# Kernel optimization log

Measured on AMD Instinct MI355X. Metric: run time of the kernel, lower is better.

The kernel has to match this reference:

```python
import jax, jax.numpy as jnp
import numpy as np

B, S, L = 256, 512, 128


def setup_inputs() -> dict:
    key = jax.random.key(0)
    k0, k1, k2, k3, k4, k5 = jax.random.split(key, 6)
    features = jax.random.normal(k0, (B, S, L), dtype=jnp.float32)
    attention_mask = jnp.ones((B, S), dtype=jnp.int32)  # all positions valid
    labels = jax.random.randint(k1, (B, S), 0, L)
    confidence = jax.random.uniform(k2, (B,), dtype=jnp.float32)
    start_transitions = jax.random.uniform(k3, (L,), minval=-0.1, maxval=0.1)
    end_transitions = jax.random.uniform(k4, (L,), minval=-0.1, maxval=0.1)
    transitions = jax.random.uniform(k5, (L, L), minval=-0.1, maxval=0.1)
    return {
        "features": features,
        "start_transitions": start_transitions,
        "end_transitions": end_transitions,
        "transitions": transitions,
        "confidence": confidence,
        "attention_mask": attention_mask,
        "labels": labels,
    }


def _crf_loss(features, start_transitions, end_transitions, transitions,
              confidence, attention_mask, labels):
    # time-major, matching torch.swapaxes(features, 0, 1)
    feats = jnp.swapaxes(features, 0, 1)                    # [S,B,L]
    mask = jnp.swapaxes(attention_mask, 0, 1).astype(bool)  # [S,B]
    labs = jnp.swapaxes(jnp.where(labels == -100, 0, labels), 0, 1)  # [S,B]
    bs = feats.shape[1]
    barange = jnp.arange(bs)

    # ---- log numerator (gold path score), fully vectorized over time ----
    emit = jnp.take_along_axis(feats, labs[:, :, None], axis=2)[..., 0]  # [S,B]
    trans_scores = transitions[labs[:-1], labs[1:]]                      # [S-1,B]
    maskf = mask[1:].astype(feats.dtype)
    log_num = (start_transitions[labs[0]] + emit[0]
               + jnp.sum((trans_scores + emit[1:]) * maskf, axis=0))
    seq_lens = mask.sum(axis=0) - 1                                      # [B]
    last_tags = labs[seq_lens, barange]
    log_num = log_num + end_transitions[last_tags]

    # ---- log denominator (partition function) via sequential scan ----
    def step(alpha, xs):
        feat_t, mask_t = xs  # [B,L], [B]
        nxt = jax.nn.logsumexp(
            alpha[:, :, None] + transitions[None, :, :] + feat_t[:, None, :],
            axis=1)
        return jnp.where(mask_t[:, None], nxt, alpha), None

    alpha0 = start_transitions + feats[0]                    # [B,L]
    alpha, _ = jax.lax.scan(step, alpha0, (feats[1:], mask[1:]))
    log_den = jax.nn.logsumexp(alpha + end_transitions, axis=1)  # [B]

    loss = (log_den - log_num) * confidence
    return jnp.mean(loss)


def reference(features, start_transitions, end_transitions, transitions,
              confidence, attention_mask, labels):
    return _crf_loss(features, start_transitions, end_transitions, transitions,
                     confidence, attention_mask, labels)
```

## Files before the change

kernel.cpp:

```cpp
#include <hip/hip_runtime.h>
#include <hip/hip_bf16.h>
#include <math.h>

#define NB 256
#define SS 512
#define LL 128

typedef short bf16x8 __attribute__((ext_vector_type(8)));
typedef float f32x4 __attribute__((ext_vector_type(4)));

__device__ __forceinline__ short f2bf(float f) {
    __hip_bfloat16 h = __float2bfloat16(f);
    short s;
    __builtin_memcpy(&s, &h, 2);
    return s;
}
__device__ __forceinline__ float bf2f(short s) {
    return __int_as_float(((int)(unsigned short)s) << 16);
}

#define MFMA1632(c, a, bb) \
    c = __builtin_amdgcn_mfma_f32_16x16x32_bf16(a, bb, c, 0, 0, 0)

__device__ __forceinline__ void wave_barrier() {
    asm volatile("s_waitcnt lgkmcnt(0)" ::: "memory");
    __builtin_amdgcn_s_barrier();
}

template <int ISB>
__device__ __forceinline__ void run_chain4(
    const int w, const int lane,
    const float* __restrict__ fb,
    const float* __restrict__ start_t,
    const float* __restrict__ end_t,
    const float* __restrict__ trans,
    short* __restrict__ img,
    float* __restrict__ eRing,
    const int* __restrict__ lmask,
    float* __restrict__ outv,
    float* __restrict__ oute)
{
    const int lo = lane & 15;
    const int hi = lane >> 4;
    const int nt0 = 2 * w, nt1 = 2 * w + 1;

    bf16x8 Af0[4], Af1[4];
#pragma unroll
    for (int kt = 0; kt < 4; ++kt) {
        bf16x8 f0, f1;
        const int n0 = 16 * nt0 + lo, n1 = 16 * nt1 + lo;
#pragma unroll
        for (int j = 0; j < 8; ++j) {
            const int k = 32 * kt + 8 * hi + j;
            f0[j] = f2bf(__expf(ISB ? trans[n0 * LL + k] : trans[k * LL + n0]));
            f1[j] = f2bf(__expf(ISB ? trans[n1 * LL + k] : trans[k * LL + n1]));
        }
        Af0[kt] = f0;
        Af1[kt] = f1;
    }

    float v[2][4];
#pragma unroll
    for (int n2 = 0; n2 < 2; ++n2)
#pragma unroll
        for (int j = 0; j < 4; ++j) {
            const int p = 16 * (2 * w + n2) + 4 * hi + j;
            v[n2][j] = ISB ? __expf(end_t[p]) : __expf(start_t[p] + fb[p]);
        }

    short4 pk0, pk1;
    {
        f32x4 e0 = {1.f, 1.f, 1.f, 1.f}, e1 = e0;
        if (ISB) {
#pragma unroll
            for (int j = 0; j < 4; ++j) {
                e0[j] = __expf(fb[(size_t)511 * LL + 16 * nt0 + 4 * hi + j]);
                e1[j] = __expf(fb[(size_t)511 * LL + 16 * nt1 + 4 * hi + j]);
            }
        }
        pk0.x = f2bf(v[0][0] * e0[0]); pk0.y = f2bf(v[0][1] * e0[1]);
        pk0.z = f2bf(v[0][2] * e0[2]); pk0.w = f2bf(v[0][3] * e0[3]);
        pk1.x = f2bf(v[1][0] * e1[0]); pk1.y = f2bf(v[1][1] * e1[1]);
        pk1.z = f2bf(v[1][2] * e1[2]); pk1.w = f2bf(v[1][3] * e1[3]);
    }

    float2 nxt;
    {
        const int row = ISB ? (508 - w) : (w + 3);
        nxt = *(const float2*)(fb + (size_t)row * LL + 2 * lane);
    }

    wave_barrier();

    int eacc = 0;

    for (int r = 0; r < 256; ++r) {
        short* ib = img + (r & 1) * LL;

        if (lo == 0) {
            *(short4*)(ib + 32 * w + 4 * hi) = pk0;
            *(short4*)(ib + 32 * w + 16 + 4 * hi) = pk1;
        }
        const float* rp = eRing + (r & 3) * LL + 4 * hi;
        f32x4 ec0 = *(const f32x4*)(rp + 16 * nt0);
        f32x4 ec1 = *(const f32x4*)(rp + 16 * nt1);
        if (w == (r & 3)) {
            *(float2*)(eRing + ((r + 2) & 3) * LL + 2 * lane) =
                make_float2(__expf(nxt.x), __expf(nxt.y));
            const int rowN = ISB ? (504 - r) : (r + 7);
            nxt = *(const float2*)(fb + (size_t)rowN * LL + 2 * lane);
        }
        int mt = lmask[ISB ? (511 - r) : (r + 1)];
        if (!ISB && r == 255) mt = 0;

        wave_barrier();

        __builtin_amdgcn_s_setprio(1);
        bf16x8 Bf[4];
#pragma unroll
        for (int kt = 0; kt < 4; ++kt)
            Bf[kt] = *(const bf16x8*)(ib + 32 * kt + 8 * hi);

        f32x4 c0a = {0.f, 0.f, 0.f, 0.f}, c0b = c0a, c1a = c0a, c1b = c0a;
        MFMA1632(c0a, Af0[0], Bf[0]);
        MFMA1632(c1a, Af1[0], Bf[0]);
        MFMA1632(c0b, Af0[2], Bf[2]);
        MFMA1632(c1b, Af1[2], Bf[2]);
        MFMA1632(c0a, Af0[1], Bf[1]);
        MFMA1632(c1a, Af1[1], Bf[1]);
        MFMA1632(c0b, Af0[3], Bf[3]);
        MFMA1632(c1b, Af1[3], Bf[3]);
        __builtin_amdgcn_s_setprio(0);
        const f32x4 cc0 = c0a + c0b;
        const f32x4 cc1 = c1a + c1b;

#pragma unroll
        for (int j = 0; j < 4; ++j) {
            const float c0 = ISB ? cc0[j] : ec0[j] * cc0[j];
            const float c1 = ISB ? cc1[j] : ec1[j] * cc1[j];
            v[0][j] = mt ? c0 : v[0][j];
            v[1][j] = mt ? c1 : v[1][j];
        }

        if ((r & 7) == 7) {
            float s = 0.f;
#pragma unroll
            for (int kt = 0; kt < 4; ++kt)
#pragma unroll
                for (int j = 0; j < 8; ++j) s += bf2f(Bf[kt][j]);
            s += __shfl_xor(s, 16);
            s += __shfl_xor(s, 32);
            int ex;
            frexpf(s, &ex);
#pragma unroll
            for (int n2 = 0; n2 < 2; ++n2)
#pragma unroll
                for (int j = 0; j < 4; ++j) v[n2][j] = ldexpf(v[n2][j], -ex);
            eacc += ex;
        }

        pk0.x = f2bf(ISB ? v[0][0] * ec0[0] : v[0][0]);
        pk0.y = f2bf(ISB ? v[0][1] * ec0[1] : v[0][1]);
        pk0.z = f2bf(ISB ? v[0][2] * ec0[2] : v[0][2]);
        pk0.w = f2bf(ISB ? v[0][3] * ec0[3] : v[0][3]);
        pk1.x = f2bf(ISB ? v[1][0] * ec1[0] : v[1][0]);
        pk1.y = f2bf(ISB ? v[1][1] * ec1[1] : v[1][1]);
        pk1.z = f2bf(ISB ? v[1][2] * ec1[2] : v[1][2]);
        pk1.w = f2bf(ISB ? v[1][3] * ec1[3] : v[1][3]);
    }

    if (lo == 0) {
        *(f32x4*)(outv + 16 * nt0 + 4 * hi) =
            (f32x4){v[0][0], v[0][1], v[0][2], v[0][3]};
        *(f32x4*)(outv + 16 * nt1 + 4 * hi) =
            (f32x4){v[1][0], v[1][1], v[1][2], v[1][3]};
    }
    if (w == 0 && lane == 0) *oute = (float)eacc;
}

__global__ __launch_bounds__(256, 2) void crf_chain_kernel(
    const float* __restrict__ feats,
    const float* __restrict__ start_t,
    const float* __restrict__ end_t,
    const float* __restrict__ trans,
    const int* __restrict__ mask,
    const int* __restrict__ labels,
    float* __restrict__ ws)
{
    const int bid = blockIdx.x;
    const int b = bid & 255;
    const int isB = bid >> 8;
    const int tid = threadIdx.x;
    const int w = tid >> 6;
    const int lane = tid & 63;

    __shared__ __align__(16) short img[2 * LL];
    __shared__ __align__(16) float eRing[4 * LL];
    __shared__ int lmask[SS];
    __shared__ float nred[4];
    __shared__ int cred[4];

    const float* fb = feats + (size_t)b * SS * LL;

    lmask[tid] = mask[b * SS + tid];
    lmask[tid + 256] = mask[b * SS + tid + 256];
    {
        const int slot = tid >> 7;
        const int e = tid & 127;
        const int row = isB ? (510 - slot) : (1 + slot);
        eRing[slot * LL + e] = __expf(fb[(size_t)row * LL + e]);
    }

    float* av = ws;
    float* bv = ws + NB * LL;
    float* eFa = ws + 2 * NB * LL;
    float* eBa = eFa + NB;
    float* lognum = eBa + NB;

    if (isB)
        run_chain4<1>(w, lane, fb, start_t, end_t, trans, img, eRing, lmask,
                      bv + b * LL, eBa + b);
    else
        run_chain4<0>(w, lane, fb, start_t, end_t, trans, img, eRing, lmask,
                      av + b * LL, eFa + b);

    if (isB) {
        const int* lb = labels + b * SS;
        const int* mb = mask + b * SS;
        float term = 0.f;
        int cnt = 0;
#pragma unroll
        for (int q = 0; q < 2; ++q) {
            const int tt = tid + 256 * q;
            int l = lb[tt];
            if ((unsigned)l >= LL) l = 0;
            const int m = mb[tt];
            cnt += (m != 0);
            if (tt == 0) {
                term += start_t[l] + fb[l];
            } else if (m) {
                int lp = lb[tt - 1];
                if ((unsigned)lp >= LL) lp = 0;
                term += trans[lp * LL + l] + fb[(size_t)tt * LL + l];
            }
        }
#pragma unroll
        for (int o = 1; o < 64; o <<= 1) {
            term += __shfl_xor(term, o);
            cnt += __shfl_xor(cnt, o);
        }
        if (lane == 0) { nred[w] = term; cred[w] = cnt; }
        __syncthreads();
        if (tid == 0) {
            const float tot = nred[0] + nred[1] + nred[2] + nred[3];
            const int c = cred[0] + cred[1] + cred[2] + cred[3];
            int sl = c - 1;
            sl = sl < 0 ? 0 : (sl >= SS ? SS - 1 : sl);
            int lt = lb[sl];
            if ((unsigned)lt >= LL) lt = 0;
            lognum[b] = tot + end_t[lt];
        }
    }
}

__global__ __launch_bounds__(256) void crf_final_kernel(
    const float* __restrict__ ws, const float* __restrict__ conf,
    float* __restrict__ out)
{
    const int tid = threadIdx.x;
    const float* av = ws;
    const float* bv = ws + NB * LL;
    const float* eFa = ws + 2 * NB * LL;
    const float* eBa = eFa + NB;
    const float* ln = eBa + NB;

    const float4* a4 = (const float4*)(av + tid * LL);
    const float4* b4 = (const float4*)(bv + tid * LL);
    float dot = 0.f;
#pragma unroll 8
    for (int k = 0; k < 32; ++k) {
        float4 a = a4[k], bb = b4[k];
        dot += a.x * bb.x + a.y * bb.y + a.z * bb.z + a.w * bb.w;
    }
    float logZ = logf(dot) + 0.69314718055994531f * (eFa[tid] + eBa[tid]);
    float loss = (logZ - ln[tid]) * conf[tid] * (1.0f / NB);

#pragma unroll
    for (int o = 1; o < 64; o <<= 1) loss += __shfl_xor(loss, o);
    __shared__ float red[4];
    if ((tid & 63) == 0) red[tid >> 6] = loss;
    __syncthreads();
    if (tid == 0) out[0] = red[0] + red[1] + red[2] + red[3];
}

extern "C" void kernel_launch(void* const* d_in, const int* in_sizes, int n_in,
                              void* d_out, int out_size, void* d_ws, size_t ws_size,
                              hipStream_t stream) {
    const float* feats  = (const float*)d_in[0];
    const float* startt = (const float*)d_in[1];
    const float* endt   = (const float*)d_in[2];
    const float* trans  = (const float*)d_in[3];
    const float* conf   = (const float*)d_in[4];
    const int*   mask   = (const int*)d_in[5];
    const int*   labels = (const int*)d_in[6];
    float* out = (float*)d_out;
    float* ws = (float*)d_ws;

    hipLaunchKernelGGL(crf_chain_kernel, dim3(2 * NB), dim3(256), 0, stream,
                       feats, startt, endt, trans, mask, labels, ws);
    hipLaunchKernelGGL(crf_final_kernel, dim3(1), dim3(256), 0, stream,
                       ws, conf, out);
}
```

Before: 214.8 us.

## Interleave two batch chains per block to hide the serial step latency

Each block now runs two independent sequences (a pair of batch items) in lockstep and alternates their scan steps. While one chain's MFMA result and bf16 repack are in flight, the other chain's LDS image is read, so the latency of each serial step is hidden. The grid is halved to 256 blocks with launch bounds of one block per SM. The transition matrix is loaded once and shared by both chains, but register pressure rises and each block does twice the serial work.

```diff
diff --git a/kernel.cpp b/kernel.cpp
--- a/kernel.cpp
+++ b/kernel.cpp
@@ -28,17 +28,22 @@
 }
 
 template <int ISB>
-__device__ __forceinline__ void run_chain4(
+__device__ __forceinline__ void run_pair(
     const int w, const int lane,
-    const float* __restrict__ fb,
+    const float* __restrict__ fb0,
+    const float* __restrict__ fb1,
     const float* __restrict__ start_t,
     const float* __restrict__ end_t,
     const float* __restrict__ trans,
-    short* __restrict__ img,
-    float* __restrict__ eRing,
-    const int* __restrict__ lmask,
+    short* __restrict__ imgA,
+    short* __restrict__ imgB,
+    float* __restrict__ ringA,
+    float* __restrict__ ringB,
+    const int* __restrict__ lmA,
+    const int* __restrict__ lmB,
     float* __restrict__ outv,
-    float* __restrict__ oute)
+    float* __restrict__ oute,
+    const int b0, const int b1)
 {
     const int lo = lane & 15;
     const int hi = lane >> 4;
@@ -59,89 +64,98 @@
         Af1[kt] = f1;
     }
 
-    float v[2][4];
+    float vA[2][4], vB[2][4];
 #pragma unroll
     for (int n2 = 0; n2 < 2; ++n2)
 #pragma unroll
         for (int j = 0; j < 4; ++j) {
             const int p = 16 * (2 * w + n2) + 4 * hi + j;
-            v[n2][j] = ISB ? __expf(end_t[p]) : __expf(start_t[p] + fb[p]);
-        }
-
-    short4 pk0, pk1;
+            vA[n2][j] = ISB ? __expf(end_t[p]) : __expf(start_t[p] + fb0[p]);
+            vB[n2][j] = ISB ? __expf(end_t[p]) : __expf(start_t[p] + fb1[p]);
+        }
+
+    short4 pkA0, pkA1, pkB0, pkB1;
     {
-        f32x4 e0 = {1.f, 1.f, 1.f, 1.f}, e1 = e0;
+        f32x4 eA0 = {1.f, 1.f, 1.f, 1.f}, eA1 = eA0, eB0 = eA0, eB1 = eA0;
         if (ISB) {
 #pragma unroll
             for (int j = 0; j < 4; ++j) {
-                e0[j] = __expf(fb[(size_t)511 * LL + 16 * nt0 + 4 * hi + j]);
-                e1[j] = __expf(fb[(size_t)511 * LL + 16 * nt1 + 4 * hi + j]);
-            }
-        }
-        pk0.x = f2bf(v[0][0] * e0[0]); pk0.y = f2bf(v[0][1] * e0[1]);
-        pk0.z = f2bf(v[0][2] * e0[2]); pk0.w = f2bf(v[0][3] * e0[3]);
-        pk1.x = f2bf(v[1][0] * e1[0]); pk1.y = f2bf(v[1][1] * e1[1]);
-        pk1.z = f2bf(v[1][2] * e1[2]); pk1.w = f2bf(v[1][3] * e1[3]);
-    }
-
-    float2 nxt;
+                eA0[j] = __expf(fb0[(size_t)511 * LL + 16 * nt0 + 4 * hi + j]);
+                eA1[j] = __expf(fb0[(size_t)511 * LL + 16 * nt1 + 4 * hi + j]);
+                eB0[j] = __expf(fb1[(size_t)511 * LL + 16 * nt0 + 4 * hi + j]);
+                eB1[j] = __expf(fb1[(size_t)511 * LL + 16 * nt1 + 4 * hi + j]);
+            }
+        }
+        pkA0.x = f2bf(vA[0][0] * eA0[0]); pkA0.y = f2bf(vA[0][1] * eA0[1]);
+        pkA0.z = f2bf(vA[0][2] * eA0[2]); pkA0.w = f2bf(vA[0][3] * eA0[3]);
+        pkA1.x = f2bf(vA[1][0] * eA1[0]); pkA1.y = f2bf(vA[1][1] * eA1[1]);
+        pkA1.z = f2bf(vA[1][2] * eA1[2]); pkA1.w = f2bf(vA[1][3] * eA1[3]);
+        pkB0.x = f2bf(vB[0][0] * eB0[0]); pkB0.y = f2bf(vB[0][1] * eB0[1]);
+        pkB0.z = f2bf(vB[0][2] * eB0[2]); pkB0.w = f2bf(vB[0][3] * eB0[3]);
+        pkB1.x = f2bf(vB[1][0] * eB1[0]); pkB1.y = f2bf(vB[1][1] * eB1[1]);
+        pkB1.z = f2bf(vB[1][2] * eB1[2]); pkB1.w = f2bf(vB[1][3] * eB1[3]);
+    }
+
+    if (lo == 0) {
+        *(short4*)(imgA + 32 * w + 4 * hi) = pkA0;
+        *(short4*)(imgA + 32 * w + 16 + 4 * hi) = pkA1;
+    }
+
+    float2 nxtA, nxtB;
     {
         const int row = ISB ? (508 - w) : (w + 3);
-        nxt = *(const float2*)(fb + (size_t)row * LL + 2 * lane);
-    }
-
-    wave_barrier();
-
-    int eacc = 0;
+        nxtA = *(const float2*)(fb0 + (size_t)row * LL + 2 * lane);
+        nxtB = *(const float2*)(fb1 + (size_t)row * LL + 2 * lane);
+    }
+
+    int eaccA = 0, eaccB = 0;
 
     for (int r = 0; r < 256; ++r) {
-        short* ib = img + (r & 1) * LL;
-
-        if (lo == 0) {
-            *(short4*)(ib + 32 * w + 4 * hi) = pk0;
-            *(short4*)(ib + 32 * w + 16 + 4 * hi) = pk1;
-        }
-        const float* rp = eRing + (r & 3) * LL + 4 * hi;
-        f32x4 ec0 = *(const f32x4*)(rp + 16 * nt0);
-        f32x4 ec1 = *(const f32x4*)(rp + 16 * nt1);
+        wave_barrier();
+        const short* ibA = imgA + (r & 1) * LL;
+        bf16x8 Bf[4];
+#pragma unroll
+        for (int kt = 0; kt < 4; ++kt)
+            Bf[kt] = *(const bf16x8*)(ibA + 32 * kt + 8 * hi);
+        {
+            short* ob = imgB + (r & 1) * LL;
+            if (lo == 0) {
+                *(short4*)(ob + 32 * w + 4 * hi) = pkB0;
+                *(short4*)(ob + 32 * w + 16 + 4 * hi) = pkB1;
+            }
+        }
+        const float* rpA = ringA + (r & 3) * LL + 4 * hi;
+        f32x4 ecA0 = *(const f32x4*)(rpA + 16 * nt0);
+        f32x4 ecA1 = *(const f32x4*)(rpA + 16 * nt1);
         if (w == (r & 3)) {
-            *(float2*)(eRing + ((r + 2) & 3) * LL + 2 * lane) =
-                make_float2(__expf(nxt.x), __expf(nxt.y));
+            *(float2*)(ringA + ((r + 2) & 3) * LL + 2 * lane) =
+                make_float2(__expf(nxtA.x), __expf(nxtA.y));
             const int rowN = ISB ? (504 - r) : (r + 7);
-            nxt = *(const float2*)(fb + (size_t)rowN * LL + 2 * lane);
-        }
-        int mt = lmask[ISB ? (511 - r) : (r + 1)];
-        if (!ISB && r == 255) mt = 0;
-
-        wave_barrier();
-
-        __builtin_amdgcn_s_setprio(1);
-        bf16x8 Bf[4];
-#pragma unroll
-        for (int kt = 0; kt < 4; ++kt)
-            Bf[kt] = *(const bf16x8*)(ib + 32 * kt + 8 * hi);
-
-        f32x4 c0a = {0.f, 0.f, 0.f, 0.f}, c0b = c0a, c1a = c0a, c1b = c0a;
-        MFMA1632(c0a, Af0[0], Bf[0]);
-        MFMA1632(c1a, Af1[0], Bf[0]);
-        MFMA1632(c0b, Af0[2], Bf[2]);
-        MFMA1632(c1b, Af1[2], Bf[2]);
-        MFMA1632(c0a, Af0[1], Bf[1]);
-        MFMA1632(c1a, Af1[1], Bf[1]);
-        MFMA1632(c0b, Af0[3], Bf[3]);
-        MFMA1632(c1b, Af1[3], Bf[3]);
-        __builtin_amdgcn_s_setprio(0);
-        const f32x4 cc0 = c0a + c0b;
-        const f32x4 cc1 = c1a + c1b;
-
-#pragma unroll
-        for (int j = 0; j < 4; ++j) {
-            const float c0 = ISB ? cc0[j] : ec0[j] * cc0[j];
-            const float c1 = ISB ? cc1[j] : ec1[j] * cc1[j];
-            v[0][j] = mt ? c0 : v[0][j];
-            v[1][j] = mt ? c1 : v[1][j];
-        }
-
+            nxtA = *(const float2*)(fb0 + (size_t)rowN * LL + 2 * lane);
+        }
+        int mtA = lmA[ISB ? (511 - r) : (r + 1)];
+        if (!ISB && r == 255) mtA = 0;
+
+        {
+            f32x4 c0a = {0.f, 0.f, 0.f, 0.f}, c0b = c0a, c1a = c0a, c1b = c0a;
+            MFMA1632(c0a, Af0[0], Bf[0]);
+            MFMA1632(c1a, Af1[0], Bf[0]);
+            MFMA1632(c0b, Af0[2], Bf[2]);
+            MFMA1632(c1b, Af1[2], Bf[2]);
+            MFMA1632(c0a, Af0[1], Bf[1]);
+            MFMA1632(c1a, Af1[1], Bf[1]);
+            MFMA1632(c0b, Af0[3], Bf[3]);
+            MFMA1632(c1b, Af1[3], Bf[3]);
+            const f32x4 cc0 = c0a + c0b;
+            const f32x4 cc1 = c1a + c1b;
+#pragma unroll
+            for (int j = 0; j < 4; ++j) {
+                const float c0 = ISB ? cc0[j] : ecA0[j] * cc0[j];
+                const float c1 = ISB ? cc1[j] : ecA1[j] * cc1[j];
+                vA[0][j] = mtA ? c0 : vA[0][j];
+                vA[1][j] = mtA ? c1 : vA[1][j];
+            }
+        }
         if ((r & 7) == 7) {
             float s = 0.f;
 #pragma unroll
@@ -155,30 +169,106 @@
 #pragma unroll
             for (int n2 = 0; n2 < 2; ++n2)
 #pragma unroll
-                for (int j = 0; j < 4; ++j) v[n2][j] = ldexpf(v[n2][j], -ex);
-            eacc += ex;
-        }
-
-        pk0.x = f2bf(ISB ? v[0][0] * ec0[0] : v[0][0]);
-        pk0.y = f2bf(ISB ? v[0][1] * ec0[1] : v[0][1]);
-        pk0.z = f2bf(ISB ? v[0][2] * ec0[2] : v[0][2]);
-        pk0.w = f2bf(ISB ? v[0][3] * ec0[3] : v[0][3]);
-        pk1.x = f2bf(ISB ? v[1][0] * ec1[0] : v[1][0]);
-        pk1.y = f2bf(ISB ? v[1][1] * ec1[1] : v[1][1]);
-        pk1.z = f2bf(ISB ? v[1][2] * ec1[2] : v[1][2]);
-        pk1.w = f2bf(ISB ? v[1][3] * ec1[3] : v[1][3]);
+                for (int j = 0; j < 4; ++j) vA[n2][j] = ldexpf(vA[n2][j], -ex);
+            eaccA += ex;
+        }
+        pkA0.x = f2bf(ISB ? vA[0][0] * ecA0[0] : vA[0][0]);
+        pkA0.y = f2bf(ISB ? vA[0][1] * ecA0[1] : vA[0][1]);
+        pkA0.z = f2bf(ISB ? vA[0][2] * ecA0[2] : vA[0][2]);
+        pkA0.w = f2bf(ISB ? vA[0][3] * ecA0[3] : vA[0][3]);
+        pkA1.x = f2bf(ISB ? vA[1][0] * ecA1[0] : vA[1][0]);
+        pkA1.y = f2bf(ISB ? vA[1][1] * ecA1[1] : vA[1][1]);
+        pkA1.z = f2bf(ISB ? vA[1][2] * ecA1[2] : vA[1][2]);
+        pkA1.w = f2bf(ISB ? vA[1][3] * ecA1[3] : vA[1][3]);
+
+        wave_barrier();
+        const short* ibB = imgB + (r & 1) * LL;
+        bf16x8 Bg[4];
+#pragma unroll
+        for (int kt = 0; kt < 4; ++kt)
+            Bg[kt] = *(const bf16x8*)(ibB + 32 * kt + 8 * hi);
+        {
+            short* ob = imgA + ((r + 1) & 1) * LL;
+            if (lo == 0) {
+                *(short4*)(ob + 32 * w + 4 * hi) = pkA0;
+                *(short4*)(ob + 32 * w + 16 + 4 * hi) = pkA1;
+            }
+        }
+        const float* rpB = ringB + (r & 3) * LL + 4 * hi;
+        f32x4 ecB0 = *(const f32x4*)(rpB + 16 * nt0);
+        f32x4 ecB1 = *(const f32x4*)(rpB + 16 * nt1);
+        if (w == (r & 3)) {
+            *(float2*)(ringB + ((r + 2) & 3) * LL + 2 * lane) =
+                make_float2(__expf(nxtB.x), __expf(nxtB.y));
+            const int rowN = ISB ? (504 - r) : (r + 7);
+            nxtB = *(const float2*)(fb1 + (size_t)rowN * LL + 2 * lane);
+        }
+        int mtB = lmB[ISB ? (511 - r) : (r + 1)];
+        if (!ISB && r == 255) mtB = 0;
+
+        {
+            f32x4 c0a = {0.f, 0.f, 0.f, 0.f}, c0b = c0a, c1a = c0a, c1b = c0a;
+            MFMA1632(c0a, Af0[0], Bg[0]);
+            MFMA1632(c1a, Af1[0], Bg[0]);
+            MFMA1632(c0b, Af0[2], Bg[2]);
+            MFMA1632(c1b, Af1[2], Bg[2]);
+            MFMA1632(c0a, Af0[1], Bg[1]);
+            MFMA1632(c1a, Af1[1], Bg[1]);
+            MFMA1632(c0b, Af0[3], Bg[3]);
+            MFMA1632(c1b, Af1[3], Bg[3]);
+            const f32x4 cc0 = c0a + c0b;
+            const f32x4 cc1 = c1a + c1b;
+#pragma unroll
+            for (int j = 0; j < 4; ++j) {
+                const float c0 = ISB ? cc0[j] : ecB0[j] * cc0[j];
+                const float c1 = ISB ? cc1[j] : ecB1[j] * cc1[j];
+                vB[0][j] = mtB ? c0 : vB[0][j];
+                vB[1][j] = mtB ? c1 : vB[1][j];
+            }
+        }
+        if ((r & 7) == 7) {
+            float s = 0.f;
+#pragma unroll
+            for (int kt = 0; kt < 4; ++kt)
+#pragma unroll
+                for (int j = 0; j < 8; ++j) s += bf2f(Bg[kt][j]);
+            s += __shfl_xor(s, 16);
+            s += __shfl_xor(s, 32);
+            int ex;
+            frexpf(s, &ex);
+#pragma unroll
+            for (int n2 = 0; n2 < 2; ++n2)
+#pragma unroll
+                for (int j = 0; j < 4; ++j) vB[n2][j] = ldexpf(vB[n2][j], -ex);
+            eaccB += ex;
+        }
+        pkB0.x = f2bf(ISB ? vB[0][0] * ecB0[0] : vB[0][0]);
+        pkB0.y = f2bf(ISB ? vB[0][1] * ecB0[1] : vB[0][1]);
+        pkB0.z = f2bf(ISB ? vB[0][2] * ecB0[2] : vB[0][2]);
+        pkB0.w = f2bf(ISB ? vB[0][3] * ecB0[3] : vB[0][3]);
+        pkB1.x = f2bf(ISB ? vB[1][0] * ecB1[0] : vB[1][0]);
+        pkB1.y = f2bf(ISB ? vB[1][1] * ecB1[1] : vB[1][1]);
+        pkB1.z = f2bf(ISB ? vB[1][2] * ecB1[2] : vB[1][2]);
+        pkB1.w = f2bf(ISB ? vB[1][3] * ecB1[3] : vB[1][3]);
     }
 
     if (lo == 0) {
-        *(f32x4*)(outv + 16 * nt0 + 4 * hi) =
-            (f32x4){v[0][0], v[0][1], v[0][2], v[0][3]};
-        *(f32x4*)(outv + 16 * nt1 + 4 * hi) =
-            (f32x4){v[1][0], v[1][1], v[1][2], v[1][3]};
-    }
-    if (w == 0 && lane == 0) *oute = (float)eacc;
-}
-
-__global__ __launch_bounds__(256, 2) void crf_chain_kernel(
+        *(f32x4*)(outv + b0 * LL + 16 * nt0 + 4 * hi) =
+            (f32x4){vA[0][0], vA[0][1], vA[0][2], vA[0][3]};
+        *(f32x4*)(outv + b0 * LL + 16 * nt1 + 4 * hi) =
+            (f32x4){vA[1][0], vA[1][1], vA[1][2], vA[1][3]};
+        *(f32x4*)(outv + b1 * LL + 16 * nt0 + 4 * hi) =
+            (f32x4){vB[0][0], vB[0][1], vB[0][2], vB[0][3]};
+        *(f32x4*)(outv + b1 * LL + 16 * nt1 + 4 * hi) =
+            (f32x4){vB[1][0], vB[1][1], vB[1][2], vB[1][3]};
+    }
+    if (w == 0 && lane == 0) {
+        oute[b0] = (float)eaccA;
+        oute[b1] = (float)eaccB;
+    }
+}
+
+__global__ __launch_bounds__(256, 1) void crf_chain_kernel(
     const float* __restrict__ feats,
     const float* __restrict__ start_t,
     const float* __restrict__ end_t,
@@ -188,27 +278,34 @@
     float* __restrict__ ws)
 {
     const int bid = blockIdx.x;
-    const int b = bid & 255;
-    const int isB = bid >> 8;
+    const int isB = bid >> 7;
+    const int p = bid & 127;
+    const int b0 = 2 * p, b1 = 2 * p + 1;
     const int tid = threadIdx.x;
     const int w = tid >> 6;
     const int lane = tid & 63;
 
-    __shared__ __align__(16) short img[2 * LL];
-    __shared__ __align__(16) float eRing[4 * LL];
-    __shared__ int lmask[SS];
+    __shared__ __align__(16) short imgA[2 * LL];
+    __shared__ __align__(16) short imgB[2 * LL];
+    __shared__ __align__(16) float ringA[4 * LL];
+    __shared__ __align__(16) float ringB[4 * LL];
+    __shared__ int lmask2[2 * SS];
     __shared__ float nred[4];
     __shared__ int cred[4];
 
-    const float* fb = feats + (size_t)b * SS * LL;
-
-    lmask[tid] = mask[b * SS + tid];
-    lmask[tid + 256] = mask[b * SS + tid + 256];
+    const float* fb0 = feats + (size_t)b0 * SS * LL;
+    const float* fb1 = feats + (size_t)b1 * SS * LL;
+
+    lmask2[tid] = mask[b0 * SS + tid];
+    lmask2[tid + 256] = mask[b0 * SS + tid + 256];
+    lmask2[SS + tid] = mask[b1 * SS + tid];
+    lmask2[SS + tid + 256] = mask[b1 * SS + tid + 256];
     {
         const int slot = tid >> 7;
         const int e = tid & 127;
         const int row = isB ? (510 - slot) : (1 + slot);
-        eRing[slot * LL + e] = __expf(fb[(size_t)row * LL + e]);
+        ringA[slot * LL + e] = __expf(fb0[(size_t)row * LL + e]);
+        ringB[slot * LL + e] = __expf(fb1[(size_t)row * LL + e]);
     }
 
     float* av = ws;
@@ -218,30 +315,32 @@
     float* lognum = eBa + NB;
 
     if (isB)
-        run_chain4<1>(w, lane, fb, start_t, end_t, trans, img, eRing, lmask,
-                      bv + b * LL, eBa + b);
+        run_pair<1>(w, lane, fb0, fb1, start_t, end_t, trans, imgA, imgB,
+                    ringA, ringB, lmask2, lmask2 + SS, bv, eBa, b0, b1);
     else
-        run_chain4<0>(w, lane, fb, start_t, end_t, trans, img, eRing, lmask,
-                      av + b * LL, eFa + b);
+        run_pair<0>(w, lane, fb0, fb1, start_t, end_t, trans, imgA, imgB,
+                    ringA, ringB, lmask2, lmask2 + SS, av, eFa, b0, b1);
 
     if (isB) {
-        const int* lb = labels + b * SS;
-        const int* mb = mask + b * SS;
+        const int bb = (w < 2) ? b0 : b1;
+        const float* fbn = (w < 2) ? fb0 : fb1;
+        const int* lb = labels + bb * SS;
+        const int* mb = mask + bb * SS;
         float term = 0.f;
         int cnt = 0;
 #pragma unroll
-        for (int q = 0; q < 2; ++q) {
-            const int tt = tid + 256 * q;
+        for (int q = 0; q < 4; ++q) {
+            const int tt = (w & 1) * 256 + lane + 64 * q;
             int l = lb[tt];
             if ((unsigned)l >= LL) l = 0;
             const int m = mb[tt];
             cnt += (m != 0);
             if (tt == 0) {
-                term += start_t[l] + fb[l];
+                term += start_t[l] + fbn[l];
             } else if (m) {
                 int lp = lb[tt - 1];
                 if ((unsigned)lp >= LL) lp = 0;
-                term += trans[lp * LL + l] + fb[(size_t)tt * LL + l];
+                term += trans[lp * LL + l] + fbn[(size_t)tt * LL + l];
             }
         }
 #pragma unroll
@@ -252,13 +351,22 @@
         if (lane == 0) { nred[w] = term; cred[w] = cnt; }
         __syncthreads();
         if (tid == 0) {
-            const float tot = nred[0] + nred[1] + nred[2] + nred[3];
-            const int c = cred[0] + cred[1] + cred[2] + cred[3];
+            const float tot = nred[0] + nred[1];
+            const int c = cred[0] + cred[1];
             int sl = c - 1;
             sl = sl < 0 ? 0 : (sl >= SS ? SS - 1 : sl);
-            int lt = lb[sl];
+            int lt = labels[b0 * SS + sl];
             if ((unsigned)lt >= LL) lt = 0;
-            lognum[b] = tot + end_t[lt];
+            lognum[b0] = tot + end_t[lt];
+        }
+        if (tid == 128) {
+            const float tot = nred[2] + nred[3];
+            const int c = cred[2] + cred[3];
+            int sl = c - 1;
+            sl = sl < 0 ? 0 : (sl >= SS ? SS - 1 : sl);
+            int lt = labels[b1 * SS + sl];
+            if ((unsigned)lt >= LL) lt = 0;
+            lognum[b1] = tot + end_t[lt];
         }
     }
 }
@@ -306,7 +414,7 @@
     float* out = (float*)d_out;
     float* ws = (float*)d_ws;
 
-    hipLaunchKernelGGL(crf_chain_kernel, dim3(2 * NB), dim3(256), 0, stream,
+    hipLaunchKernelGGL(crf_chain_kernel, dim3(NB), dim3(256), 0, stream,
                        feats, startt, endt, trans, mask, labels, ws);
     hipLaunchKernelGGL(crf_final_kernel, dim3(1), dim3(256), 0, stream,
                        ws, conf, out);
```

After: 296.8 us. 1.38x slower.
